# Kernel optimization log

Hardware: AMD Instinct MI355X
Metric: run time of the kernel (lower is better)

## Reference

```python
import jax, jax.numpy as jnp
import numpy as np

E, D, F, K = 8, 1024, 4096, 2  # num_experts, embed_dim, intermediate_dim, top_k


def new_gelu(x):
    # NewGELUActivation: 0.5*x*(1+tanh(sqrt(2/pi)*(x+0.044715*x^3)))
    c = jnp.sqrt(2.0 / jnp.pi).astype(x.dtype)
    return 0.5 * x * (1.0 + jnp.tanh(c * (x + 0.044715 * x * x * x)))


def setup_inputs() -> dict:
    key = jax.random.key(0)
    ks = jax.random.split(key, 6)
    std = 0.02
    return {
        "hidden_states": jax.random.normal(ks[0], (4, 2048, D), dtype=jnp.float32),
        "gate_w": jax.random.normal(ks[1], (E, D), dtype=jnp.float32) * std,   # Linear(out=E,in=D), no bias
        "w_fc": jax.random.normal(ks[2], (E, F, D), dtype=jnp.float32) * std,  # per-expert c_fc weight [out,in]
        "b_fc": jnp.zeros((E, F), dtype=jnp.float32),
        "w_proj": jax.random.normal(ks[3], (E, D, F), dtype=jnp.float32) * std,
        "b_proj": jnp.zeros((E, D), dtype=jnp.float32),
    }


def reference(hidden_states, gate_w, w_fc, b_fc, w_proj, b_proj):
    B, S, _ = hidden_states.shape
    x = hidden_states.reshape(-1, D)                       # [T, D]
    T = x.shape[0]
    logits = x @ gate_w.T                                  # [T, E]
    topk_vals, topk_idx = jax.lax.top_k(logits, K)         # [T, K]
    topk_w = jax.nn.softmax(topk_vals, axis=-1)            # [T, K]
    # scatter top-k weights into a dense [T, E] sparse-weight matrix
    sparse_w = jnp.zeros((T, E), dtype=x.dtype).at[
        jnp.arange(T)[:, None], topk_idx
    ].set(topk_w)
    # per-expert dense MLP, combined with (mostly-zero) routing weights.
    # Mathematically identical to gather->MLP->scatter in the original
    # (dropout is identity in eval mode).
    out = jnp.zeros_like(x)
    for e in range(E):
        h = new_gelu(x @ w_fc[e].T + b_fc[e])              # [T, F]
        y = h @ w_proj[e].T + b_proj[e]                    # [T, D]
        out = out + y * sparse_w[:, e:e + 1]
    return out.reshape(B, S, D)
```

## Files before the change

### kernel.cpp

```cpp
#include <hip/hip_runtime.h>
#include <hip/hip_bf16.h>

#define E_ 8
#define D_ 1024
#define F_ 4096
#define K_ 2
#define ALIGN_ 128

typedef __attribute__((ext_vector_type(8))) short short8;
typedef __attribute__((ext_vector_type(4))) float f32x4;

__device__ __forceinline__ unsigned f2bf(float f){
  union { __hip_bfloat16 h; unsigned short u; } c;
  c.h = __float2bfloat16(f);
  return (unsigned)c.u;
}

__device__ __forceinline__ float bf2f(unsigned u){
  union { float f; unsigned u; } c;
  c.u = u << 16;
  return c.f;
}

__device__ __forceinline__ float gelu_f(float v){
  const float c0 = 0.7978845608028654f;
  float z = c0 * (v + 0.044715f * v * v * v);
  float e = __expf(2.0f * z);
  float t = 1.0f - 2.0f / (1.0f + e);
  return 0.5f * v * (1.0f + t);
}

__device__ __forceinline__ void gload16(const void* gsrc, void* ldst){
  __builtin_amdgcn_global_load_lds(
      (const __attribute__((address_space(1))) unsigned int*)gsrc,
      (__attribute__((address_space(3))) unsigned int*)ldst, 16, 0, 0);
}

__global__ void gate_kernel(const float* __restrict__ x, const float* __restrict__ gw,
                            int* __restrict__ tidx, float* __restrict__ tw,
                            unsigned short* __restrict__ x16, int T){
  int wid = threadIdx.x >> 6, lane = threadIdx.x & 63;
  int t = blockIdx.x * 4 + wid;
  if (t >= T) return;
  const float4* xr = reinterpret_cast<const float4*>(x + (size_t)t * D_);
  uint2* x16r = reinterpret_cast<uint2*>(x16 + (size_t)t * D_);
  double acc[E_];
  #pragma unroll
  for (int e = 0; e < E_; ++e) acc[e] = 0.0;
  #pragma unroll
  for (int j = 0; j < 4; ++j){
    float4 xv = xr[j*64 + lane];
    uint2 p;
    p.x = f2bf(xv.x) | (f2bf(xv.y) << 16);
    p.y = f2bf(xv.z) | (f2bf(xv.w) << 16);
    x16r[j*64 + lane] = p;
    #pragma unroll
    for (int e = 0; e < E_; ++e){
      float4 wv = *reinterpret_cast<const float4*>(gw + (size_t)e*D_ + (j*64 + lane)*4);
      acc[e] += (double)xv.x*wv.x + (double)xv.y*wv.y + (double)xv.z*wv.z + (double)xv.w*wv.w;
    }
  }
  #pragma unroll
  for (int e = 0; e < E_; ++e){
    #pragma unroll
    for (int off = 32; off >= 1; off >>= 1)
      acc[e] += __shfl_xor(acc[e], off);
  }
  if (lane == 0){
    float l[E_];
    #pragma unroll
    for (int e = 0; e < E_; ++e) l[e] = (float)acc[e];
    int i0 = 0; float v0 = l[0];
    #pragma unroll
    for (int e = 1; e < E_; ++e) if (l[e] > v0){ v0 = l[e]; i0 = e; }
    int i1 = -1; float v1 = -1e30f;
    #pragma unroll
    for (int e = 0; e < E_; ++e) if (e != i0 && l[e] > v1){ v1 = l[e]; i1 = e; }
    float e1 = expf(v1 - v0);
    float s = 1.0f + e1;
    tidx[2*t] = i0; tidx[2*t+1] = i1;
    tw[2*t] = 1.0f / s; tw[2*t+1] = e1 / s;
  }
}

__global__ void slotscan_kernel(const int* __restrict__ tidx, int* __restrict__ counts,
                                int* __restrict__ tokSlot, int nAssign){
  __shared__ int cnt[256][E_];
  __shared__ int wtot[E_][4];
  __shared__ int ebase[E_];
  const int tid = threadIdx.x;
  const int lane = tid & 63, w = tid >> 6;
  const int per = (nAssign + 255) >> 8;
  const int base = tid * per;

  #pragma unroll
  for (int e = 0; e < E_; ++e) cnt[tid][e] = 0;
  for (int j = 0; j < per; ++j){
    int i = base + j;
    if (i < nAssign) cnt[tid][tidx[i]]++;
  }
  int excl[E_];
  #pragma unroll
  for (int e = 0; e < E_; ++e){
    int v = cnt[tid][e];
    int s = v;
    #pragma unroll
    for (int off = 1; off < 64; off <<= 1){
      int u = __shfl_up(s, off);
      if (lane >= off) s += u;
    }
    if (lane == 63) wtot[e][w] = s;
    excl[e] = s - v;
  }
  __syncthreads();
  if (tid == 0){
    int pre = 0;
    #pragma unroll
    for (int e = 0; e < E_; ++e){
      int tot = 0;
      #pragma unroll
      for (int ww = 0; ww < 4; ++ww){ int c = wtot[e][ww]; wtot[e][ww] = tot; tot += c; }
      counts[e] = tot;
      ebase[e] = pre;
      pre += (tot + (ALIGN_-1)) & ~(ALIGN_-1);
    }
  }
  __syncthreads();
  #pragma unroll
  for (int e = 0; e < E_; ++e)
    cnt[tid][e] = ebase[e] + wtot[e][w] + excl[e];
  for (int j = 0; j < per; ++j){
    int i = base + j;
    if (i < nAssign){
      int e = tidx[i];
      tokSlot[i] = cnt[tid][e]++;
    }
  }
}

__global__ void scatgath_kernel(const unsigned short* __restrict__ x16,
                                const int* __restrict__ tokSlot,
                                __hip_bfloat16* __restrict__ Abuf){
  int t = blockIdx.x;
  int s0 = tokSlot[K_*t], s1 = tokSlot[K_*t + 1];
  uint4 p = *(reinterpret_cast<const uint4*>(x16 + (size_t)t * D_) + threadIdx.x);
  *(reinterpret_cast<uint4*>(reinterpret_cast<unsigned short*>(Abuf) + (size_t)s0*D_) + threadIdx.x) = p;
  *(reinterpret_cast<uint4*>(reinterpret_cast<unsigned short*>(Abuf) + (size_t)s1*D_) + threadIdx.x) = p;
}

__global__ void cvtw_kernel(const float* __restrict__ src, __hip_bfloat16* __restrict__ dst, int n4){
  int stride = gridDim.x * blockDim.x;
  for (int i = blockIdx.x * blockDim.x + threadIdx.x; i < n4; i += stride){
    float4 v = reinterpret_cast<const float4*>(src)[i];
    uint2 p;
    p.x = f2bf(v.x) | (f2bf(v.y) << 16);
    p.y = f2bf(v.z) | (f2bf(v.w) << 16);
    reinterpret_cast<uint2*>(dst)[i] = p;
  }
}

__global__ void combine_kernel(const unsigned short* __restrict__ Ybuf,
                               const int* __restrict__ tidx, const float* __restrict__ tw,
                               const int* __restrict__ tokSlot,
                               const float* __restrict__ bpj,
                               float* __restrict__ out){
  int t = blockIdx.x;
  int d = threadIdx.x * 4;
  int e0 = tidx[2*t], e1 = tidx[2*t+1];
  float w0 = tw[2*t], w1 = tw[2*t+1];
  int s0 = tokSlot[2*t], s1 = tokSlot[2*t+1];
  uint2 ya = *reinterpret_cast<const uint2*>(Ybuf + (size_t)s0*D_ + d);
  uint2 yb = *reinterpret_cast<const uint2*>(Ybuf + (size_t)s1*D_ + d);
  float4 b0 = *reinterpret_cast<const float4*>(bpj + (size_t)e0*D_ + d);
  float4 b1 = *reinterpret_cast<const float4*>(bpj + (size_t)e1*D_ + d);
  float4 r;
  r.x = w0*(bf2f(ya.x & 0xffffu) + b0.x) + w1*(bf2f(yb.x & 0xffffu) + b1.x);
  r.y = w0*(bf2f(ya.x >> 16)     + b0.y) + w1*(bf2f(yb.x >> 16)     + b1.y);
  r.z = w0*(bf2f(ya.y & 0xffffu) + b0.z) + w1*(bf2f(yb.y & 0xffffu) + b1.z);
  r.w = w0*(bf2f(ya.y >> 16)     + b0.w) + w1*(bf2f(yb.y >> 16)     + b1.w);
  *reinterpret_cast<float4*>(out + (size_t)t*D_ + d) = r;
}

template<bool WB16, bool PH1>
__global__ __launch_bounds__(256, 4) void gemm_kernel(
    const __hip_bfloat16* __restrict__ Abuf,
    const void* __restrict__ W,
    const float* __restrict__ bias,
    const int* __restrict__ counts,
    unsigned short* __restrict__ Out16)
{
  constexpr int KA = PH1 ? D_ : F_;
  constexpr int NT = PH1 ? F_ : D_;
  constexpr int NK = KA / 64;
  constexpr int NX = NT / 128;

  __shared__ char sA[128*128];
  __shared__ char sB[128*128];

  int pre[E_]; int total = 0;
  #pragma unroll
  for (int i = 0; i < E_; ++i){ pre[i] = total; total += (counts[i] + (ALIGN_-1)) & ~(ALIGN_-1); }

  int q = gridDim.x >> 3;
  int wgid = (blockIdx.x & 7) * q + (blockIdx.x >> 3);
  int yt = wgid / NX, xt = wgid - yt*NX;
  int rowBase = yt * 128;
  if (rowBase >= total) return;
  int e = 0;
  #pragma unroll
  for (int i = 1; i < E_; ++i) if (rowBase >= pre[i]) e = i;
  int nBase = xt * 128;

  const int tid = threadIdx.x;
  const int wid = tid >> 6, lane = tid & 63;
  const int lr = lane & 15, lg = lane >> 4;
  const int wr = wid >> 1, wc = wid & 1;

  const unsigned short* Wb = (const unsigned short*)W;
  const float* Wf = (const float*)W;
  const size_t Wrow0 = (size_t)e * NT + nBase;

  f32x4 acc[4][4];
  #pragma unroll
  for (int m = 0; m < 4; ++m)
    #pragma unroll
    for (int n = 0; n < 4; ++n) acc[m][n] = (f32x4){0.f,0.f,0.f,0.f};

  for (int kt = 0; kt < NK; ++kt){
    int k0 = kt * 64;
    #pragma unroll
    for (int i = 0; i < 4; ++i){
      int flat = i*4096 + wid*1024 + lane*16;
      int row  = flat >> 7;
      int colb = flat & 127;
      int scol = colb ^ ((row & 7) << 4);
      const char* src = (const char*)(Abuf + (size_t)(rowBase + row) * KA + k0) + scol;
      gload16(src, sA + i*4096 + wid*1024);
    }
    if constexpr (WB16){
      #pragma unroll
      for (int i = 0; i < 4; ++i){
        int flat = i*4096 + wid*1024 + lane*16;
        int row  = flat >> 7;
        int colb = flat & 127;
        int scol = colb ^ ((row & 7) << 4);
        const char* src = (const char*)(Wb + (Wrow0 + row) * KA + k0) + scol;
        gload16(src, sB + i*4096 + wid*1024);
      }
    } else {
      #pragma unroll
      for (int i = 0; i < 8; ++i){
        int f4  = i*256 + tid;
        int row = f4 >> 4;
        int c4  = f4 & 15;
        float4 v = *reinterpret_cast<const float4*>(Wf + (Wrow0 + row) * KA + k0 + c4*4);
        uint2 p;
        p.x = f2bf(v.x) | (f2bf(v.y) << 16);
        p.y = f2bf(v.z) | (f2bf(v.w) << 16);
        int byte = row*128 + c4*8;
        *reinterpret_cast<uint2*>(sB + (byte ^ ((row & 7) << 4))) = p;
      }
    }
    __syncthreads();
    #pragma unroll
    for (int ks = 0; ks < 2; ++ks){
      short8 a[4], b[4];
      #pragma unroll
      for (int m = 0; m < 4; ++m){
        int row = wr*64 + m*16 + lr;
        a[m] = *reinterpret_cast<const short8*>(sA + row*128 + ((ks*64 + lg*16) ^ ((row & 7) << 4)));
      }
      #pragma unroll
      for (int n = 0; n < 4; ++n){
        int row = wc*64 + n*16 + lr;
        b[n] = *reinterpret_cast<const short8*>(sB + row*128 + ((ks*64 + lg*16) ^ ((row & 7) << 4)));
      }
      #pragma unroll
      for (int m = 0; m < 4; ++m)
        #pragma unroll
        for (int n = 0; n < 4; ++n)
          acc[m][n] = __builtin_amdgcn_mfma_f32_16x16x32_bf16(b[n], a[m], acc[m][n], 0, 0, 0);
    }
    __syncthreads();
  }

  int colBase = nBase + wc*64;
  if constexpr (PH1){
    #pragma unroll
    for (int n = 0; n < 4; ++n){
      int gc = colBase + n*16 + lg*4;
      float4 b4 = *reinterpret_cast<const float4*>(bias + (size_t)e*F_ + gc);
      #pragma unroll
      for (int m = 0; m < 4; ++m){
        int gr = rowBase + wr*64 + m*16 + lr;
        uint2 p;
        p.x = f2bf(gelu_f(acc[m][n][0] + b4.x)) | (f2bf(gelu_f(acc[m][n][1] + b4.y)) << 16);
        p.y = f2bf(gelu_f(acc[m][n][2] + b4.z)) | (f2bf(gelu_f(acc[m][n][3] + b4.w)) << 16);
        *reinterpret_cast<uint2*>(Out16 + (size_t)gr * F_ + gc) = p;
      }
    }
  } else {
    #pragma unroll
    for (int n = 0; n < 4; ++n){
      int gc = colBase + n*16 + lg*4;
      #pragma unroll
      for (int m = 0; m < 4; ++m){
        int gr = rowBase + wr*64 + m*16 + lr;
        uint2 p;
        p.x = f2bf(acc[m][n][0]) | (f2bf(acc[m][n][1]) << 16);
        p.y = f2bf(acc[m][n][2]) | (f2bf(acc[m][n][3]) << 16);
        *reinterpret_cast<uint2*>(Out16 + (size_t)gr * D_ + gc) = p;
      }
    }
  }
}

extern "C" void kernel_launch(void* const* d_in, const int* in_sizes, int n_in,
                              void* d_out, int out_size, void* d_ws, size_t ws_size,
                              hipStream_t stream){
  const float* x   = (const float*)d_in[0];
  const float* gw  = (const float*)d_in[1];
  const float* wfc = (const float*)d_in[2];
  const float* bfc = (const float*)d_in[3];
  const float* wpj = (const float*)d_in[4];
  const float* bpj = (const float*)d_in[5];
  float* out = (float*)d_out;

  int T = in_sizes[0] / D_;
  int nAssign = T * K_;
  int nSlotsMax = nAssign + E_ * ALIGN_;
  int rowTiles = nSlotsMax / 128;

  char* ws = (char*)d_ws;
  size_t o = 0;
  int*   tidx    = (int*)(ws + o); o += (size_t)nAssign * 4;
  float* tw      = (float*)(ws + o); o += (size_t)nAssign * 4;
  int*   counts  = (int*)(ws + o); o += 256;
  int*   tokSlot = (int*)(ws + o); o += (size_t)nAssign * 4;
  o = (o + 255) & ~(size_t)255;

  size_t abytes = (size_t)nSlotsMax * D_ * 2;
  size_t hbytes = (size_t)nSlotsMax * F_ * 2;
  size_t wbytes = (size_t)E_ * F_ * D_ * 2;

  __hip_bfloat16* Abuf = (__hip_bfloat16*)(ws + o); o += abytes;
  __hip_bfloat16* Hbuf = (__hip_bfloat16*)(ws + o); o += hbytes;
  size_t o_w = o;
  __hip_bfloat16* wA = (__hip_bfloat16*)(ws + o_w);
  __hip_bfloat16* wB = (__hip_bfloat16*)(ws + o_w + wbytes);

  unsigned short* x16 = (unsigned short*)Hbuf;

  bool newPath = (ws_size >= o_w + 2*wbytes);
  bool midPath = (ws_size >= o_w + wbytes);

  int n4 = E_ * F_ * D_ / 4;
  int nwg1 = (F_/128) * rowTiles;
  int nwg2 = (D_/128) * rowTiles;
  unsigned short* Ybuf = (unsigned short*)Abuf;

  gate_kernel<<<(T + 3)/4, 256, 0, stream>>>(x, gw, tidx, tw, x16, T);
  slotscan_kernel<<<1, 256, 0, stream>>>(tidx, counts, tokSlot, nAssign);
  scatgath_kernel<<<T, 128, 0, stream>>>(x16, tokSlot, Abuf);

  if (newPath){
    cvtw_kernel<<<2048, 256, 0, stream>>>(wfc, wA, n4);
    cvtw_kernel<<<2048, 256, 0, stream>>>(wpj, wB, n4);
    gemm_kernel<true, true><<<nwg1, 256, 0, stream>>>(
        Abuf, (const void*)wA, bfc, counts, (unsigned short*)Hbuf);
    gemm_kernel<true, false><<<nwg2, 256, 0, stream>>>(
        Hbuf, (const void*)wB, bpj, counts, Ybuf);
  } else if (midPath){
    cvtw_kernel<<<2048, 256, 0, stream>>>(wfc, wA, n4);
    gemm_kernel<true, true><<<nwg1, 256, 0, stream>>>(
        Abuf, (const void*)wA, bfc, counts, (unsigned short*)Hbuf);
    cvtw_kernel<<<2048, 256, 0, stream>>>(wpj, wA, n4);
    gemm_kernel<true, false><<<nwg2, 256, 0, stream>>>(
        Hbuf, (const void*)wA, bpj, counts, Ybuf);
  } else {
    gemm_kernel<false, true><<<nwg1, 256, 0, stream>>>(
        Abuf, (const void*)wfc, bfc, counts, (unsigned short*)Hbuf);
    gemm_kernel<false, false><<<nwg2, 256, 0, stream>>>(
        Hbuf, (const void*)wpj, bpj, counts, Ybuf);
  }
  combine_kernel<<<T, 256, 0, stream>>>(Ybuf, tidx, tw, tokSlot, bpj, out);
}
```

Baseline: 524.6 us.

## Fold weight conversions into gate and first GEMM launches to overlap work

The fp32-to-bf16 conversion of w_fc is fused into the gate kernel launch as extra blocks, and the w_proj conversion is appended as extra blocks to the first expert GEMM launch. This removes two standalone launches and lets the memory-bound conversion run alongside the compute-bound GEMM and the small gate work. The risk is that conversion blocks compete with GEMM tiles for CUs and bandwidth, and the block scheduling order may delay GEMM tiles. The GEMM tile swizzle now uses nwgGemm instead of gridDim.

New measurement: 506.7 us. 1.04x faster.

```diff
diff --git a/kernel.cpp b/kernel.cpp
--- a/kernel.cpp
+++ b/kernel.cpp
@@ -36,9 +36,28 @@
       (__attribute__((address_space(3))) unsigned int*)ldst, 16, 0, 0);
 }
 
-__global__ void gate_kernel(const float* __restrict__ x, const float* __restrict__ gw,
-                            int* __restrict__ tidx, float* __restrict__ tw,
-                            unsigned short* __restrict__ x16, int T){
+__device__ __forceinline__ void cvt_range(const float* __restrict__ src,
+                                          __hip_bfloat16* __restrict__ dst,
+                                          int n4, int cb, int nCvt){
+  size_t stride = (size_t)nCvt * 256;
+  for (size_t i = (size_t)cb*256 + threadIdx.x; i < (size_t)n4; i += stride){
+    float4 v = reinterpret_cast<const float4*>(src)[i];
+    uint2 p;
+    p.x = f2bf(v.x) | (f2bf(v.y) << 16);
+    p.y = f2bf(v.z) | (f2bf(v.w) << 16);
+    reinterpret_cast<uint2*>(dst)[i] = p;
+  }
+}
+
+__global__ void gatecvt_kernel(const float* __restrict__ x, const float* __restrict__ gw,
+                               int* __restrict__ tidx, float* __restrict__ tw,
+                               unsigned short* __restrict__ x16, int T,
+                               const float* __restrict__ csrc, __hip_bfloat16* __restrict__ cdst,
+                               int n4, int gateBlocks){
+  if ((int)blockIdx.x >= gateBlocks){
+    cvt_range(csrc, cdst, n4, blockIdx.x - gateBlocks, gridDim.x - gateBlocks);
+    return;
+  }
   int wid = threadIdx.x >> 6, lane = threadIdx.x & 63;
   int t = blockIdx.x * 4 + wid;
   if (t >= T) return;
@@ -149,14 +168,7 @@
 }
 
 __global__ void cvtw_kernel(const float* __restrict__ src, __hip_bfloat16* __restrict__ dst, int n4){
-  int stride = gridDim.x * blockDim.x;
-  for (int i = blockIdx.x * blockDim.x + threadIdx.x; i < n4; i += stride){
-    float4 v = reinterpret_cast<const float4*>(src)[i];
-    uint2 p;
-    p.x = f2bf(v.x) | (f2bf(v.y) << 16);
-    p.y = f2bf(v.z) | (f2bf(v.w) << 16);
-    reinterpret_cast<uint2*>(dst)[i] = p;
-  }
+  cvt_range(src, dst, n4, blockIdx.x, gridDim.x);
 }
 
 __global__ void combine_kernel(const unsigned short* __restrict__ Ybuf,
@@ -187,7 +199,10 @@
     const void* __restrict__ W,
     const float* __restrict__ bias,
     const int* __restrict__ counts,
-    unsigned short* __restrict__ Out16)
+    unsigned short* __restrict__ Out16,
+    const float* __restrict__ csrc,
+    __hip_bfloat16* __restrict__ cdst,
+    int n4, int nwgGemm)
 {
   constexpr int KA = PH1 ? D_ : F_;
   constexpr int NT = PH1 ? F_ : D_;
@@ -197,11 +212,16 @@
   __shared__ char sA[128*128];
   __shared__ char sB[128*128];
 
+  if ((int)blockIdx.x >= nwgGemm){
+    cvt_range(csrc, cdst, n4, blockIdx.x - nwgGemm, gridDim.x - nwgGemm);
+    return;
+  }
+
   int pre[E_]; int total = 0;
   #pragma unroll
   for (int i = 0; i < E_; ++i){ pre[i] = total; total += (counts[i] + (ALIGN_-1)) & ~(ALIGN_-1); }
 
-  int q = gridDim.x >> 3;
+  int q = nwgGemm >> 3;
   int wgid = (blockIdx.x & 7) * q + (blockIdx.x >> 3);
   int yt = wgid / NX, xt = wgid - yt*NX;
   int rowBase = yt * 128;
@@ -357,31 +377,39 @@
   int n4 = E_ * F_ * D_ / 4;
   int nwg1 = (F_/128) * rowTiles;
   int nwg2 = (D_/128) * rowTiles;
+  int gateBlocks = (T + 3)/4;
   unsigned short* Ybuf = (unsigned short*)Abuf;
 
-  gate_kernel<<<(T + 3)/4, 256, 0, stream>>>(x, gw, tidx, tw, x16, T);
-  slotscan_kernel<<<1, 256, 0, stream>>>(tidx, counts, tokSlot, nAssign);
-  scatgath_kernel<<<T, 128, 0, stream>>>(x16, tokSlot, Abuf);
-
   if (newPath){
-    cvtw_kernel<<<2048, 256, 0, stream>>>(wfc, wA, n4);
-    cvtw_kernel<<<2048, 256, 0, stream>>>(wpj, wB, n4);
+    gatecvt_kernel<<<gateBlocks + 2048, 256, 0, stream>>>(
+        x, gw, tidx, tw, x16, T, wfc, wA, n4, gateBlocks);
+    slotscan_kernel<<<1, 256, 0, stream>>>(tidx, counts, tokSlot, nAssign);
+    scatgath_kernel<<<T, 128, 0, stream>>>(x16, tokSlot, Abuf);
+    gemm_kernel<true, true><<<nwg1 + 2048, 256, 0, stream>>>(
+        Abuf, (const void*)wA, bfc, counts, (unsigned short*)Hbuf, wpj, wB, n4, nwg1);
+    gemm_kernel<true, false><<<nwg2, 256, 0, stream>>>(
+        Hbuf, (const void*)wB, bpj, counts, Ybuf, nullptr, nullptr, 0, nwg2);
+    combine_kernel<<<T, 256, 0, stream>>>(Ybuf, tidx, tw, tokSlot, bpj, out);
+  } else if (midPath){
+    gatecvt_kernel<<<gateBlocks + 2048, 256, 0, stream>>>(
+        x, gw, tidx, tw, x16, T, wfc, wA, n4, gateBlocks);
+    slotscan_kernel<<<1, 256, 0, stream>>>(tidx, counts, tokSlot, nAssign);
+    scatgath_kernel<<<T, 128, 0, stream>>>(x16, tokSlot, Abuf);
     gemm_kernel<true, true><<<nwg1, 256, 0, stream>>>(
-        Abuf, (const void*)wA, bfc, counts, (unsigned short*)Hbuf);
-    gemm_kernel<true, false><<<nwg2, 256, 0, stream>>>(
-        Hbuf, (const void*)wB, bpj, counts, Ybuf);
-  } else if (midPath){
-    cvtw_kernel<<<2048, 256, 0, stream>>>(wfc, wA, n4);
-    gemm_kernel<true, true><<<nwg1, 256, 0, stream>>>(
-        Abuf, (const void*)wA, bfc, counts, (unsigned short*)Hbuf);
+        Abuf, (const void*)wA, bfc, counts, (unsigned short*)Hbuf, nullptr, nullptr, 0, nwg1);
     cvtw_kernel<<<2048, 256, 0, stream>>>(wpj, wA, n4);
     gemm_kernel<true, false><<<nwg2, 256, 0, stream>>>(
-        Hbuf, (const void*)wA, bpj, counts, Ybuf);
+        Hbuf, (const void*)wA, bpj, counts, Ybuf, nullptr, nullptr, 0, nwg2);
+    combine_kernel<<<T, 256, 0, stream>>>(Ybuf, tidx, tw, tokSlot, bpj, out);
   } else {
+    gatecvt_kernel<<<gateBlocks, 256, 0, stream>>>(
+        x, gw, tidx, tw, x16, T, nullptr, nullptr, 0, gateBlocks);
+    slotscan_kernel<<<1, 256, 0, stream>>>(tidx, counts, tokSlot, nAssign);
+    scatgath_kernel<<<T, 128, 0, stream>>>(x16, tokSlot, Abuf);
     gemm_kernel<false, true><<<nwg1, 256, 0, stream>>>(
-        Abuf, (const void*)wfc, bfc, counts, (unsigned short*)Hbuf);
+        Abuf, (const void*)wfc, bfc, counts, (unsigned short*)Hbuf, nullptr, nullptr, 0, nwg1);
     gemm_kernel<false, false><<<nwg2, 256, 0, stream>>>(
-        Hbuf, (const void*)wpj, bpj, counts, Ybuf);
-  }
-  combine_kernel<<<T, 256, 0, stream>>>(Ybuf, tidx, tw, tokSlot, bpj, out);
-}
+        Hbuf, (const void*)wpj, bpj, counts, Ybuf, nullptr, nullptr, 0, nwg2);
+    combine_kernel<<<T, 256, 0, stream>>>(Ybuf, tidx, tw, tokSlot, bpj, out);
+  }
+}
```
